# Kernel optimization log

Hardware: AMD Instinct MI355X
Metric: run time of the kernel (lower is better)

The kernel has to match this reference:

```python
import jax, jax.numpy as jnp
import numpy as np

N = 30000          # num nodes
E = 480000         # num edges (avg degree 16)
K = 3              # Chebyshev filter order
IN = 128           # input feature dim
LAMBDA_MAX = 2.0   # PyG default spectral bound
DIMS = [IN, 16, 32, 64, 128, 256, 512]


def setup_inputs() -> dict:
    key = jax.random.key(0)
    ks = jax.random.split(key, 20)
    inp = {
        "x": jax.random.normal(ks[0], (N, IN), dtype=jnp.float32),
        "edge_index": jax.random.randint(ks[1], (2, E), 0, N, dtype=jnp.int32),
        "edge_weight": jax.random.uniform(ks[2], (E,), dtype=jnp.float32),
        "batch": jnp.arange(N, dtype=jnp.int32),  # each node its own graph -> pooling is identity
    }
    for i in range(6):
        fi, fo = DIMS[i], DIMS[i + 1]
        scale = 1.0 / np.sqrt(fi * K)
        inp[f"W{i+1}"] = jax.random.normal(ks[3 + 2 * i], (K, fi, fo), dtype=jnp.float32) * scale
        inp[f"b{i+1}"] = jnp.zeros((fo,), dtype=jnp.float32)
    inp["fc_w"] = jax.random.normal(ks[16], (512, 3), dtype=jnp.float32) * 0.05
    inp["fc_b"] = jnp.zeros((3,), dtype=jnp.float32)
    return inp


def _cheb_conv(x, row, col, w_off, diag, W, b):
    """ChebConv with rw-normalized, rescaled Laplacian Lhat = 2L/lmax - I.
    Lhat @ v = scatter(w_off * v[row] -> col) + diag * v."""
    def lmv(v):
        return jax.ops.segment_sum(w_off[:, None] * v[row], col, num_segments=N) + diag * v
    Tx0 = x
    out = Tx0 @ W[0]
    Tx1 = lmv(x)
    out = out + Tx1 @ W[1]
    for k in range(2, W.shape[0]):
        Tx2 = 2.0 * lmv(Tx1) - Tx0
        out = out + Tx2 @ W[k]
        Tx0, Tx1 = Tx1, Tx2
    return out + b


def _forward(x, edge_index, edge_weight, batch, Ws, bs, fc_w, fc_b):
    row, col = edge_index[0], edge_index[1]
    # random-walk Laplacian L = I - D^{-1} A, then Lhat = 2L/lmax - I
    deg = jax.ops.segment_sum(edge_weight, row, num_segments=N)
    deg_inv = jnp.where(deg > 0, 1.0 / deg, 0.0)
    w_off = -(2.0 / LAMBDA_MAX) * deg_inv[row] * edge_weight   # off-diagonal entries of Lhat
    diag = 2.0 / LAMBDA_MAX - 1.0                               # diagonal entry of Lhat (0 for lmax=2)
    h = x
    for W, b in zip(Ws, bs):
        h = _cheb_conv(h, row, col, w_off, diag, W, b)
        h = jax.ops.segment_max(h, batch, num_segments=N)  # global_max_pool; identity since batch=arange
        h = jax.nn.softplus(h)
    return h @ fc_w + fc_b


def reference(x, edge_index, edge_weight, batch, W1, b1, W2, b2, W3, b3, W4, b4, W5, b5, W6, b6, fc_w, fc_b):
    Ws = [W1, W2, W3, W4, W5, W6]
    bs = [b1, b2, b3, b4, b5, b6]
    return _forward(x, edge_index, edge_weight, batch, Ws, bs, fc_w, fc_b)
```

## Files before the change

### kernel.cpp

```cpp
#include <hip/hip_runtime.h>
#include <math.h>
#include <stdint.h>

#define NN 30000
#define EE 480000
#define MPAD 30080
#define SCAN_B 30

typedef __attribute__((ext_vector_type(8))) short short8;
typedef __attribute__((ext_vector_type(4))) float floatx4;

__device__ __forceinline__ float b2f(ushort u) {
    union { uint u; float f; } c; c.u = ((uint)u) << 16; return c.f;
}
__device__ __forceinline__ ushort f2b(float f) {
    union { float f; uint u; } c; c.f = f;
    uint u = c.u;
    uint r = (u + 0x7FFFu + ((u >> 16) & 1u)) >> 16;
    return (ushort)r;
}
__device__ __forceinline__ float softplus_f(float x) {
    float a = fabsf(x) * 1.44269504f;
    float t = __builtin_amdgcn_exp2f(-a);
    float l = __builtin_amdgcn_logf(1.f + t);
    return fmaxf(x, 0.f) + 0.69314718f * l;
}

__device__ __forceinline__ void gld_lds16(const void* g, void* lds) {
    __builtin_amdgcn_global_load_lds(
        (__attribute__((address_space(1))) void*)(uintptr_t)(g),
        (__attribute__((address_space(3))) void*)(uint32_t)(uintptr_t)(lds),
        16, 0, 0);
}

__global__ void edge_pass1(const int* __restrict__ row, const int* __restrict__ col,
                           const float* __restrict__ ew,
                           float* __restrict__ deg, int* __restrict__ counts, int E) {
    int e = blockIdx.x * blockDim.x + threadIdx.x;
    if (e >= E) return;
    atomicAdd(&deg[row[e]], ew[e]);
    atomicAdd(&counts[col[e]], 1);
}

__global__ __launch_bounds__(256) void scan_part(const int* __restrict__ counts,
                                                 int* __restrict__ bsums, int N) {
    __shared__ int s[256];
    int t = threadIdx.x;
    int base = blockIdx.x * 1024 + t * 4;
    int4 v = make_int4(0, 0, 0, 0);
    if (base + 3 < N) v = *(const int4*)(counts + base);
    else {
        if (base + 0 < N) v.x = counts[base + 0];
        if (base + 1 < N) v.y = counts[base + 1];
        if (base + 2 < N) v.z = counts[base + 2];
        if (base + 3 < N) v.w = counts[base + 3];
    }
    s[t] = v.x + v.y + v.z + v.w;
    __syncthreads();
    for (int off = 1; off < 256; off <<= 1) {
        int x = (t >= off) ? s[t - off] : 0;
        __syncthreads();
        s[t] += x;
        __syncthreads();
    }
    if (t == 255) bsums[blockIdx.x] = s[255];
}

__global__ void scan_tops(int* __restrict__ bsums) {
    int lane = threadIdx.x & 63;
    int orig = (lane < SCAN_B) ? bsums[lane] : 0;
    int v = orig;
    #pragma unroll
    for (int off = 1; off < 64; off <<= 1) {
        int x = __shfl_up(v, off);
        if (lane >= off) v += x;
    }
    if (lane < SCAN_B) bsums[lane] = v - orig;
}

__global__ __launch_bounds__(256) void scan_final(
        const int* __restrict__ counts, const int* __restrict__ bsums,
        int* __restrict__ offs, int* __restrict__ cursor, int N) {
    __shared__ int s[256];
    int t = threadIdx.x;
    int base = blockIdx.x * 1024 + t * 4;
    int4 v = make_int4(0, 0, 0, 0);
    if (base + 3 < N) v = *(const int4*)(counts + base);
    else {
        if (base + 0 < N) v.x = counts[base + 0];
        if (base + 1 < N) v.y = counts[base + 1];
        if (base + 2 < N) v.z = counts[base + 2];
        if (base + 3 < N) v.w = counts[base + 3];
    }
    int sum = v.x + v.y + v.z + v.w;
    s[t] = sum;
    __syncthreads();
    for (int off = 1; off < 256; off <<= 1) {
        int x = (t >= off) ? s[t - off] : 0;
        __syncthreads();
        s[t] += x;
        __syncthreads();
    }
    int tb = s[t] - sum + bsums[blockIdx.x];
    int4 o;
    o.x = tb;
    o.y = o.x + v.x;
    o.z = o.y + v.y;
    o.w = o.z + v.z;
    if (base + 3 < N) {
        *(int4*)(offs + base) = o;
        *(int4*)(cursor + base) = o;
    } else {
        if (base + 0 < N) { offs[base + 0] = o.x; cursor[base + 0] = o.x; }
        if (base + 1 < N) { offs[base + 1] = o.y; cursor[base + 1] = o.y; }
        if (base + 2 < N) { offs[base + 2] = o.z; cursor[base + 2] = o.z; }
        if (base + 3 < N) { offs[base + 3] = o.w; cursor[base + 3] = o.w; }
    }
    if (blockIdx.x == 0 && t == 0) offs[N] = EE;
}

__global__ void edge_pass2(const int* __restrict__ row, const int* __restrict__ col,
                           const float* __restrict__ ew, const float* __restrict__ deg,
                           int* __restrict__ cursor,
                           int* __restrict__ csr_row, float* __restrict__ csr_w, int E) {
    int e = blockIdx.x * blockDim.x + threadIdx.x;
    if (e >= E) return;
    int r = row[e];
    float d = deg[r];
    float wv = (d > 0.f) ? (-ew[e] / d) : 0.f;
    int pos = atomicAdd(&cursor[col[e]], 1);
    csr_row[pos] = r;
    csr_w[pos] = wv;
}

__global__ void copy_x_kernel(const float* __restrict__ x, ushort* __restrict__ out,
                              int total4) {
    int idx = blockIdx.x * blockDim.x + threadIdx.x;
    if (idx >= total4) return;
    float4 v = *(const float4*)(x + idx * 4);
    ushort4 o;
    o.x = f2b(v.x); o.y = f2b(v.y); o.z = f2b(v.z); o.w = f2b(v.w);
    *(ushort4*)(out + idx * 4) = o;
}

__global__ void wconv_all(const float* __restrict__ W1, const float* __restrict__ W2,
                          const float* __restrict__ W3, const float* __restrict__ W4,
                          const float* __restrict__ W5, const float* __restrict__ W6,
                          ushort* __restrict__ B1, ushort* __restrict__ B2,
                          ushort* __restrict__ B3, ushort* __restrict__ B4,
                          ushort* __restrict__ B5, ushort* __restrict__ B6) {
    int idx = blockIdx.x * blockDim.x + threadIdx.x;
    if (idx < 6144) {
        int row = idx >> 7, k = idx & 127;
        int j = row >> 4, n = row & 15;
        B1[idx] = f2b(W1[(j * 128 + k) * 16 + n]);
    } else if (idx < 8192) {
        int t = idx - 6144; int n = t >> 6, k = t & 63;
        B2[t] = f2b(k < 48 ? W2[k * 32 + n] : 0.f);
    } else if (idx < 14336) {
        int t = idx - 8192; int n = t / 96, k = t - n * 96;
        B3[t] = f2b(W3[k * 64 + n]);
    } else if (idx < 38912) {
        int t = idx - 14336; int n = t / 192, k = t - n * 192;
        B4[t] = f2b(W4[k * 128 + n]);
    } else if (idx < 137216) {
        int t = idx - 38912; int n = t / 384, k = t - n * 384;
        B5[t] = f2b(W5[k * 256 + n]);
    } else if (idx < 530432) {
        int t = idx - 137216; int n = t / 768, k = t - n * 768;
        B6[t] = f2b(W6[k * 512 + n]);
    }
}

template <int FI>
__global__ __launch_bounds__(256) void lmv_bf16(
        const ushort* __restrict__ A, ushort* __restrict__ Out,
        const ushort* __restrict__ Sub, int ldi, int ldo,
        const int* __restrict__ offs, const int* __restrict__ rows,
        const float* __restrict__ w, float scale, int N) {
    constexpr int NPW = 64 / FI;
    int wave = threadIdx.x >> 6;
    int lane = threadIdx.x & 63;
    int sub = lane / FI;
    int fbase = lane & (FI - 1);
    int node = blockIdx.x * (4 * NPW) + wave * NPW + sub;
    if (node >= N) return;
    int e0 = offs[node], e1 = offs[node + 1];
    float acc[4];
    #pragma unroll
    for (int c = 0; c < 4; ++c) acc[c] = 0.f;
    int e = e0;
    for (; e + 4 <= e1; e += 4) {
        int r0 = rows[e], r1 = rows[e + 1], r2 = rows[e + 2], r3 = rows[e + 3];
        float w0 = w[e], w1 = w[e + 1], w2 = w[e + 2], w3 = w[e + 3];
        acc[0] += w0 * b2f(A[(size_t)r0 * ldi + fbase]);
        acc[1] += w1 * b2f(A[(size_t)r1 * ldi + fbase]);
        acc[2] += w2 * b2f(A[(size_t)r2 * ldi + fbase]);
        acc[3] += w3 * b2f(A[(size_t)r3 * ldi + fbase]);
    }
    for (; e < e1; ++e)
        acc[0] += w[e] * b2f(A[(size_t)rows[e] * ldi + fbase]);
    float a = (acc[0] + acc[1]) + (acc[2] + acc[3]);
    ushort* o = Out + (size_t)node * ldo + fbase;
    if (Sub) {
        const ushort* s = Sub + (size_t)node * ldo + fbase;
        *o = f2b(scale * a - b2f(*s));
    } else {
        *o = f2b(scale * a);
    }
}

__global__ __launch_bounds__(256) void lmv_l1_final(
        const ushort* __restrict__ Z,
        const ushort* __restrict__ Y,
        const float* __restrict__ b,
        ushort* __restrict__ Out,
        const int* __restrict__ offs, const int* __restrict__ rows,
        const float* __restrict__ w, int N) {
    int wave = threadIdx.x >> 6;
    int lane = threadIdx.x & 63;
    int sub = lane >> 4, f = lane & 15;
    int node = blockIdx.x * 16 + wave * 4 + sub;
    if (node >= N) return;
    int e0 = offs[node], e1 = offs[node + 1];
    const ushort* Z2 = Z + 16;
    float acc[4];
    #pragma unroll
    for (int c = 0; c < 4; ++c) acc[c] = 0.f;
    int e = e0;
    for (; e + 4 <= e1; e += 4) {
        int r0 = rows[e], r1 = rows[e + 1], r2 = rows[e + 2], r3 = rows[e + 3];
        float w0 = w[e], w1 = w[e + 1], w2 = w[e + 2], w3 = w[e + 3];
        acc[0] += w0 * b2f(Z2[(size_t)r0 * 32 + f]);
        acc[1] += w1 * b2f(Z2[(size_t)r1 * 32 + f]);
        acc[2] += w2 * b2f(Z2[(size_t)r2 * 32 + f]);
        acc[3] += w3 * b2f(Z2[(size_t)r3 * 32 + f]);
    }
    for (; e < e1; ++e)
        acc[0] += w[e] * b2f(Z2[(size_t)rows[e] * 32 + f]);
    float z3 = (acc[0] + acc[1]) + (acc[2] + acc[3]);
    float y0 = b2f(Y[(size_t)node * 48 + f]);
    float y2 = b2f(Y[(size_t)node * 48 + 32 + f]);
    float z1 = b2f(Z[(size_t)node * 32 + f]);
    float v = y0 + z1 + 2.f * z3 - y2 + b[f];
    Out[(size_t)node * 64 + f] = f2b(softplus_f(v));
}

template <int VEC>
__global__ __launch_bounds__(256) void lmv_vec(
        const ushort* __restrict__ A, ushort* __restrict__ Out,
        const ushort* __restrict__ Sub, int ld,
        const int* __restrict__ offs, const int* __restrict__ rows,
        const float* __restrict__ w, float scale) {
    constexpr int CH = 8;
    int node = blockIdx.x * 4 + (threadIdx.x >> 6);
    int lane = threadIdx.x & 63;
    int fbase = lane * VEC;
    int e0 = __builtin_amdgcn_readfirstlane(offs[node]);
    int e1 = __builtin_amdgcn_readfirstlane(offs[node + 1]);
    float acc[CH][VEC];
    #pragma unroll
    for (int c = 0; c < CH; ++c)
        #pragma unroll
        for (int v = 0; v < VEC; ++v) acc[c][v] = 0.f;
    int e = e0;
    for (; e + CH <= e1; e += CH) {
        #pragma unroll
        for (int c = 0; c < CH; ++c) {
            int r = rows[e + c];
            float we = w[e + c];
            const ushort* pr = A + (size_t)r * ld + fbase;
            if constexpr (VEC == 4) {
                ushort4 u = *(const ushort4*)pr;
                acc[c][0] += we * b2f(u.x); acc[c][1] += we * b2f(u.y);
                acc[c][2] += we * b2f(u.z); acc[c][3] += we * b2f(u.w);
            } else if constexpr (VEC == 2) {
                ushort2 u = *(const ushort2*)pr;
                acc[c][0] += we * b2f(u.x); acc[c][1] += we * b2f(u.y);
            } else {
                acc[c][0] += we * b2f(*pr);
            }
        }
    }
    for (; e < e1; ++e) {
        int c = e & (CH - 1);
        int r = rows[e];
        float we = w[e];
        const ushort* pr = A + (size_t)r * ld + fbase;
        if constexpr (VEC == 4) {
            ushort4 u = *(const ushort4*)pr;
            acc[c][0] += we * b2f(u.x); acc[c][1] += we * b2f(u.y);
            acc[c][2] += we * b2f(u.z); acc[c][3] += we * b2f(u.w);
        } else if constexpr (VEC == 2) {
            ushort2 u = *(const ushort2*)pr;
            acc[c][0] += we * b2f(u.x); acc[c][1] += we * b2f(u.y);
        } else {
            acc[c][0] += we * b2f(*pr);
        }
    }
    #pragma unroll
    for (int c = 1; c < CH; ++c)
        #pragma unroll
        for (int v = 0; v < VEC; ++v) acc[0][v] += acc[c][v];
    ushort* o = Out + (size_t)node * ld + fbase;
    if (Sub) {
        const ushort* s = Sub + (size_t)node * ld + fbase;
        ushort tmp[VEC];
        #pragma unroll
        for (int v = 0; v < VEC; ++v) tmp[v] = f2b(scale * acc[0][v] - b2f(s[v]));
        #pragma unroll
        for (int v = 0; v < VEC; ++v) o[v] = tmp[v];
    } else {
        #pragma unroll
        for (int v = 0; v < VEC; ++v) o[v] = f2b(scale * acc[0][v]);
    }
}

template <int BN, bool ACT = true>
__global__ __launch_bounds__(256) void gemm_mfma(
        const ushort* __restrict__ A, int lda, int K,
        const ushort* __restrict__ Bt,
        const float* __restrict__ bias,
        ushort* __restrict__ Out, int ldo) {
    constexpr int BM = 128, BK = 32;
    constexpr int WR = 4;
    constexpr int SM = BM / WR;
    constexpr int SN = BN;
    constexpr int FM = SM / 16;
    constexpr int FN = SN / 16;
    constexpr int CB = BN / 16;
    __shared__ __align__(16) ushort As[BM][BK];
    __shared__ __align__(16) ushort Bs[BN][BK];
    int tid = threadIdx.x;
    int wv = tid >> 6, ln = tid & 63;
    int q = ln >> 4, r16 = ln & 15;
    int m0 = blockIdx.x * BM;

    int lrow = ln >> 2;
    int gseg = (ln & 3) ^ ((ln >> 3) & 3);
    const ushort* Abase = A + (size_t)(m0 + lrow) * lda + gseg * 8;
    const ushort* Bbase = Bt + (size_t)lrow * K + gseg * 8;

    floatx4 acc[FM][FN];
    #pragma unroll
    for (int i = 0; i < FM; ++i)
        #pragma unroll
        for (int j = 0; j < FN; ++j) acc[i][j] = (floatx4){0.f, 0.f, 0.f, 0.f};

    int sw = (q ^ ((r16 >> 1) & 3)) * 8;
    int aoff[FM], boff[FN];
    #pragma unroll
    for (int i = 0; i < FM; ++i) aoff[i] = (wv * SM + i * 16 + r16) * BK + sw;
    #pragma unroll
    for (int j = 0; j < FN; ++j) boff[j] = (j * 16 + r16) * BK + sw;
    const ushort* ldsA = &As[0][0];
    const ushort* ldsB = &Bs[0][0];

    for (int k0 = 0; k0 < K; k0 += BK) {
        gld_lds16(Abase + (size_t)(wv * 16) * lda + k0, &As[wv * 16][0]);
        gld_lds16(Abase + (size_t)(64 + wv * 16) * lda + k0, &As[64 + wv * 16][0]);
        if constexpr (CB == 4) {
            gld_lds16(Bbase + (size_t)(wv * 16) * K + k0, &Bs[wv * 16][0]);
        } else {
            if (wv < CB) gld_lds16(Bbase + (size_t)(wv * 16) * K + k0, &Bs[wv * 16][0]);
        }
        __syncthreads();
        short8 af[FM], bf[FN];
        #pragma unroll
        for (int i = 0; i < FM; ++i) af[i] = *(const short8*)(ldsA + aoff[i]);
        #pragma unroll
        for (int j = 0; j < FN; ++j) bf[j] = *(const short8*)(ldsB + boff[j]);
        #pragma unroll
        for (int i = 0; i < FM; ++i)
            #pragma unroll
            for (int j = 0; j < FN; ++j)
                acc[i][j] = __builtin_amdgcn_mfma_f32_16x16x32_bf16(
                    af[i], bf[j], acc[i][j], 0, 0, 0);
        __syncthreads();
    }
    #pragma unroll
    for (int i = 0; i < FM; ++i) {
        #pragma unroll
        for (int j = 0; j < FN; ++j) {
            int n = j * 16 + r16;
            float bv = ACT ? bias[n] : 0.f;
            #pragma unroll
            for (int r = 0; r < 4; ++r) {
                int m = m0 + wv * SM + i * 16 + q * 4 + r;
                float v = acc[i][j][r] + bv;
                Out[(size_t)m * ldo + n] = f2b(ACT ? softplus_f(v) : v);
            }
        }
    }
}

template <bool FC = false, int YB = 0>
__global__ __launch_bounds__(256) void gemm_bk64(
        const ushort* __restrict__ A, int lda, int K,
        const ushort* __restrict__ Bt,
        const float* __restrict__ bias,
        ushort* __restrict__ Out, int ldo,
        const float* __restrict__ fcw, float* __restrict__ fcout) {
    constexpr int BM = 128, BN = 128, BK = 64;
    __shared__ __align__(16) ushort As[BM][BK];
    __shared__ __align__(16) ushort Bs[BN][BK];
    int tid = threadIdx.x;
    int wv = tid >> 6, ln = tid & 63;
    int wm = wv & 1, wn = wv >> 1;
    int q = ln >> 4, r16 = ln & 15;
    int yb = blockIdx.x & ((1 << YB) - 1);
    int xb = blockIdx.x >> YB;
    int m0 = xb * BM;
    int n0 = yb * BN;

    int lrow8 = ln >> 3, slds = ln & 7;
    int gseg = slds ^ lrow8;
    const ushort* Abase = A + (size_t)(m0 + lrow8) * lda + gseg * 8;
    const ushort* Bbase = Bt + (size_t)(n0 + lrow8) * K + gseg * 8;

    floatx4 acc[4][4];
    #pragma unroll
    for (int i = 0; i < 4; ++i)
        #pragma unroll
        for (int j = 0; j < 4; ++j) acc[i][j] = (floatx4){0.f, 0.f, 0.f, 0.f};

    int r7 = r16 & 7;
    int aoff[2][4], boff[2][4];
    #pragma unroll
    for (int s = 0; s < 2; ++s) {
        int segp = ((s * 4 + q) ^ r7) * 8;
        #pragma unroll
        for (int i = 0; i < 4; ++i) {
            aoff[s][i] = (wm * 64 + i * 16 + r16) * BK + segp;
            boff[s][i] = (wn * 64 + i * 16 + r16) * BK + segp;
        }
    }
    const ushort* ldsA = &As[0][0];
    const ushort* ldsB = &Bs[0][0];

    for (int k0 = 0; k0 < K; k0 += BK) {
        #pragma unroll
        for (int g = 0; g < 4; ++g)
            gld_lds16(Abase + (size_t)(wv * 8 + g * 32) * lda + k0,
                      &As[wv * 8 + g * 32][0]);
        #pragma unroll
        for (int g = 0; g < 4; ++g)
            gld_lds16(Bbase + (size_t)(wv * 8 + g * 32) * K + k0,
                      &Bs[wv * 8 + g * 32][0]);
        __syncthreads();
        #pragma unroll
        for (int s = 0; s < 2; ++s) {
            short8 af[4], bf[4];
            #pragma unroll
            for (int i = 0; i < 4; ++i) af[i] = *(const short8*)(ldsA + aoff[s][i]);
            #pragma unroll
            for (int j = 0; j < 4; ++j) bf[j] = *(const short8*)(ldsB + boff[s][j]);
            #pragma unroll
            for (int i = 0; i < 4; ++i)
                #pragma unroll
                for (int j = 0; j < 4; ++j)
                    acc[i][j] = __builtin_amdgcn_mfma_f32_16x16x32_bf16(
                        af[i], bf[j], acc[i][j], 0, 0, 0);
        }
        __syncthreads();
    }

    if constexpr (FC) {
        int pb = yb * 2 + wn;
        #pragma unroll
        for (int i = 0; i < 4; ++i) {
            #pragma unroll
            for (int r = 0; r < 4; ++r) {
                float p0 = 0.f, p1 = 0.f, p2 = 0.f;
                #pragma unroll
                for (int j = 0; j < 4; ++j) {
                    int n = n0 + wn * 64 + j * 16 + r16;
                    float v = softplus_f(acc[i][j][r] + bias[n]);
                    p0 += v * fcw[n * 3 + 0];
                    p1 += v * fcw[n * 3 + 1];
                    p2 += v * fcw[n * 3 + 2];
                }
                #pragma unroll
                for (int off = 1; off < 16; off <<= 1) {
                    p0 += __shfl_xor(p0, off);
                    p1 += __shfl_xor(p1, off);
                    p2 += __shfl_xor(p2, off);
                }
                if (r16 == 0) {
                    int m = m0 + wm * 64 + i * 16 + q * 4 + r;
                    float* dst = fcout + ((size_t)pb * MPAD + m) * 3;
                    dst[0] = p0; dst[1] = p1; dst[2] = p2;
                }
            }
        }
    } else {
        #pragma unroll
        for (int i = 0; i < 4; ++i) {
            #pragma unroll
            for (int j = 0; j < 4; ++j) {
                int n = n0 + wn * 64 + j * 16 + r16;
                float bv = bias[n];
                #pragma unroll
                for (int r = 0; r < 4; ++r) {
                    int m = m0 + wm * 64 + i * 16 + q * 4 + r;
                    Out[(size_t)m * ldo + n] = f2b(softplus_f(acc[i][j][r] + bv));
                }
            }
        }
    }
}

__global__ __launch_bounds__(256) void fc_reduce(
        const float* __restrict__ part, const float* __restrict__ fcb,
        float* __restrict__ out) {
    int idx = blockIdx.x * blockDim.x + threadIdx.x;
    if (idx >= NN * 3) return;
    int c = idx - (idx / 3) * 3;
    float s = 0.f;
    #pragma unroll
    for (int pb = 0; pb < 8; ++pb)
        s += part[(size_t)pb * MPAD * 3 + idx];
    out[idx] = s + fcb[c];
}

static inline size_t align256(size_t x) { return (x + 255) & ~(size_t)255; }

extern "C" void kernel_launch(void* const* d_in, const int* in_sizes, int n_in,
                              void* d_out, int out_size, void* d_ws, size_t ws_size,
                              hipStream_t stream) {
    const float* x   = (const float*)d_in[0];
    const int*   ei  = (const int*)d_in[1];
    const float* ew  = (const float*)d_in[2];
    const float* W[6]  = { (const float*)d_in[4],  (const float*)d_in[6],
                           (const float*)d_in[8],  (const float*)d_in[10],
                           (const float*)d_in[12], (const float*)d_in[14] };
    const float* Bv[6] = { (const float*)d_in[5],  (const float*)d_in[7],
                           (const float*)d_in[9],  (const float*)d_in[11],
                           (const float*)d_in[13], (const float*)d_in[15] };
    const float* fc_w = (const float*)d_in[16];
    const float* fc_b = (const float*)d_in[17];
    float* out = (float*)d_out;

    const int* e_row = ei;
    const int* e_col = ei + EE;

    const int fi_arr[5]   = { 16, 32, 64, 128, 256 };
    const int fo_arr[5]   = { 32, 64, 128, 256, 512 };
    const int Kpad_arr[5] = { 64, 96, 192, 384, 768 };
    const int ldo_arr[5]  = { 96, 192, 384, 768, 512 };

    char* p = (char*)d_ws;
    float* deg    = (float*)p; p += align256((size_t)NN * 4);
    int*   counts = (int*)p;   p += align256((size_t)NN * 4);
    int*   offs   = (int*)p;   p += align256((size_t)(NN + 1) * 4);
    int*   cursor = (int*)p;   p += align256((size_t)NN * 4);
    int*   bsums  = (int*)p;   p += align256((size_t)SCAN_B * 4);
    int*   csr_r  = (int*)p;   p += align256((size_t)EE * 4);
    float* csr_w  = (float*)p; p += align256((size_t)EE * 4);
    ushort* Bt1   = (ushort*)p; p += align256((size_t)48 * 128 * 2);
    ushort* Bt[5];
    for (int L = 0; L < 5; ++L) {
        Bt[L] = (ushort*)p;
        p += align256((size_t)fo_arr[L] * Kpad_arr[L] * 2);
    }
    float* fcpart = (float*)p; p += align256((size_t)8 * MPAD * 3 * 4);
    ushort* xb   = (ushort*)p; p += align256((size_t)MPAD * 128 * 2);
    ushort* Ybuf = (ushort*)p; p += align256((size_t)MPAD * 48 * 2);
    ushort* Zbuf = (ushort*)p; p += align256((size_t)MPAD * 32 * 2);
    ushort* buf0 = (ushort*)p; p += align256((size_t)MPAD * 768 * 2);
    ushort* buf1 = (ushort*)p; p += align256((size_t)MPAD * 768 * 2);
    (void)ws_size; (void)n_in; (void)in_sizes; (void)out_size;

    hipMemsetAsync(deg, 0, align256((size_t)NN * 4) + (size_t)NN * 4, stream);

    {
        int blocks = (EE + 255) / 256;
        edge_pass1<<<blocks, 256, 0, stream>>>(e_row, e_col, ew, deg, counts, EE);
        scan_part<<<SCAN_B, 256, 0, stream>>>(counts, bsums, NN);
        scan_tops<<<1, 64, 0, stream>>>(bsums);
        scan_final<<<SCAN_B, 256, 0, stream>>>(counts, bsums, offs, cursor, NN);
        edge_pass2<<<blocks, 256, 0, stream>>>(e_row, e_col, ew, deg, cursor, csr_r, csr_w, EE);
    }

    wconv_all<<<(530432 + 255) / 256, 256, 0, stream>>>(
        W[0], W[1], W[2], W[3], W[4], W[5],
        Bt1, Bt[0], Bt[1], Bt[2], Bt[3], Bt[4]);

    copy_x_kernel<<<(NN * 128 / 4 + 255) / 256, 256, 0, stream>>>(x, xb, NN * 128 / 4);

    gemm_mfma<48, false><<<dim3(MPAD / 128), 256, 0, stream>>>(
        xb, 128, 128, Bt1, nullptr, Ybuf, 48);
    lmv_bf16<32><<<(NN + 7) / 8, 256, 0, stream>>>(
        Ybuf + 16, Zbuf, nullptr, 48, 32, offs, csr_r, csr_w, 1.0f, NN);
    lmv_l1_final<<<(NN + 15) / 16, 256, 0, stream>>>(
        Zbuf, Ybuf, Bv[0], buf1, offs, csr_r, csr_w, NN);

    ushort* Abuf[5] = { buf1, buf0, buf1, buf0, buf1 };
    ushort* Obuf[5] = { buf0, buf1, buf0, buf1, buf0 };

    for (int L = 0; L < 5; ++L) {
        int fi = fi_arr[L];
        int ldA = Kpad_arr[L];
        int ldO = ldo_arr[L];
        ushort* A = Abuf[L];
        ushort* O = Obuf[L];

        switch (fi) {
            case 16:
                lmv_bf16<16><<<(NN + 15) / 16, 256, 0, stream>>>(
                    A, A + fi, nullptr, ldA, ldA, offs, csr_r, csr_w, 1.0f, NN);
                lmv_bf16<16><<<(NN + 15) / 16, 256, 0, stream>>>(
                    A + fi, A + 2 * fi, A, ldA, ldA, offs, csr_r, csr_w, 2.0f, NN);
                break;
            case 32:
                lmv_bf16<32><<<(NN + 7) / 8, 256, 0, stream>>>(
                    A, A + fi, nullptr, ldA, ldA, offs, csr_r, csr_w, 1.0f, NN);
                lmv_bf16<32><<<(NN + 7) / 8, 256, 0, stream>>>(
                    A + fi, A + 2 * fi, A, ldA, ldA, offs, csr_r, csr_w, 2.0f, NN);
                break;
            case 64:
                lmv_vec<1><<<NN / 4, 256, 0, stream>>>(
                    A, A + fi, nullptr, ldA, offs, csr_r, csr_w, 1.0f);
                lmv_vec<1><<<NN / 4, 256, 0, stream>>>(
                    A + fi, A + 2 * fi, A, ldA, offs, csr_r, csr_w, 2.0f);
                break;
            case 128:
                lmv_vec<2><<<NN / 4, 256, 0, stream>>>(
                    A, A + fi, nullptr, ldA, offs, csr_r, csr_w, 1.0f);
                lmv_vec<2><<<NN / 4, 256, 0, stream>>>(
                    A + fi, A + 2 * fi, A, ldA, offs, csr_r, csr_w, 2.0f);
                break;
            default:
                lmv_vec<4><<<NN / 4, 256, 0, stream>>>(
                    A, A + fi, nullptr, ldA, offs, csr_r, csr_w, 1.0f);
                lmv_vec<4><<<NN / 4, 256, 0, stream>>>(
                    A + fi, A + 2 * fi, A, ldA, offs, csr_r, csr_w, 2.0f);
                break;
        }

        int K = Kpad_arr[L];
        switch (fo_arr[L]) {
            case 32:
                gemm_mfma<32><<<dim3(MPAD / 128), 256, 0, stream>>>(
                    A, ldA, K, Bt[L], Bv[L + 1], O, ldO);
                break;
            case 64:
                gemm_mfma<64><<<dim3(MPAD / 128), 256, 0, stream>>>(
                    A, ldA, K, Bt[L], Bv[L + 1], O, ldO);
                break;
            case 128:
                gemm_bk64<false, 0><<<dim3(MPAD / 128), 256, 0, stream>>>(
                    A, ldA, K, Bt[L], Bv[L + 1], O, ldO, nullptr, nullptr);
                break;
            case 256:
                gemm_bk64<false, 1><<<dim3(MPAD / 128 * 2), 256, 0, stream>>>(
                    A, ldA, K, Bt[L], Bv[L + 1], O, ldO, nullptr, nullptr);
                break;
            default:
                gemm_bk64<true, 2><<<dim3(MPAD / 128 * 4), 256, 0, stream>>>(
                    A, ldA, K, Bt[L], Bv[L + 1], nullptr, 0, fc_w, fcpart);
                break;
        }
    }

    fc_reduce<<<(NN * 3 + 255) / 256, 256, 0, stream>>>(fcpart, fc_b, out);
}
```

Baseline: 489.2 us.

## Double-buffer LDS tiles in MFMA GEMMs and widen lmv edge unroll

Both MFMA GEMM kernels now keep two LDS buffers and issue the direct-to-LDS global loads for the next K tile before computing the current one. Raw s_barrier and s_waitcnt vmcnt control when each tile is consumed, so load latency can overlap with MFMA work. The sparse Laplacian kernel also accumulates 16 edges per chunk instead of 8, giving more loads in flight. In exchange, LDS use doubles, register pressure rises, and correctness depends on the hand-counted vmcnt values matching the compiler's instruction emission.

New measurement: 909.3 us. 85.9% more time.

```diff
diff --git a/kernel.cpp b/kernel.cpp
--- a/kernel.cpp
+++ b/kernel.cpp
@@ -31,6 +31,18 @@
         (__attribute__((address_space(1))) void*)(uintptr_t)(g),
         (__attribute__((address_space(3))) void*)(uint32_t)(uintptr_t)(lds),
         16, 0, 0);
+}
+
+__device__ __forceinline__ void barrier_raw() {
+    __asm__ volatile("s_barrier" ::: "memory");
+}
+template <int N>
+__device__ __forceinline__ void waitcnt_vm() {
+    if constexpr (N == 0) __asm__ volatile("s_waitcnt vmcnt(0)" ::: "memory");
+    else if constexpr (N == 2) __asm__ volatile("s_waitcnt vmcnt(2)" ::: "memory");
+    else if constexpr (N == 3) __asm__ volatile("s_waitcnt vmcnt(3)" ::: "memory");
+    else if constexpr (N == 4) __asm__ volatile("s_waitcnt vmcnt(4)" ::: "memory");
+    else if constexpr (N == 8) __asm__ volatile("s_waitcnt vmcnt(8)" ::: "memory");
 }
 
 __global__ void edge_pass1(const int* __restrict__ row, const int* __restrict__ col,
@@ -252,7 +264,7 @@
         const ushort* __restrict__ Sub, int ld,
         const int* __restrict__ offs, const int* __restrict__ rows,
         const float* __restrict__ w, float scale) {
-    constexpr int CH = 8;
+    constexpr int CH = 16;
     int node = blockIdx.x * 4 + (threadIdx.x >> 6);
     int lane = threadIdx.x & 63;
     int fbase = lane * VEC;
@@ -323,14 +335,13 @@
         const float* __restrict__ bias,
         ushort* __restrict__ Out, int ldo) {
     constexpr int BM = 128, BK = 32;
-    constexpr int WR = 4;
-    constexpr int SM = BM / WR;
-    constexpr int SN = BN;
-    constexpr int FM = SM / 16;
-    constexpr int FN = SN / 16;
+    constexpr int SM = 32;
+    constexpr int FM = 2;
+    constexpr int FN = BN / 16;
     constexpr int CB = BN / 16;
-    __shared__ __align__(16) ushort As[BM][BK];
-    __shared__ __align__(16) ushort Bs[BN][BK];
+    constexpr int WAITN = (BN == 64) ? 3 : 2;
+    __shared__ __align__(16) ushort As[2][BM][BK];
+    __shared__ __align__(16) ushort Bs[2][BN][BK];
     int tid = threadIdx.x;
     int wv = tid >> 6, ln = tid & 63;
     int q = ln >> 4, r16 = ln & 15;
@@ -353,18 +364,19 @@
     for (int i = 0; i < FM; ++i) aoff[i] = (wv * SM + i * 16 + r16) * BK + sw;
     #pragma unroll
     for (int j = 0; j < FN; ++j) boff[j] = (j * 16 + r16) * BK + sw;
-    const ushort* ldsA = &As[0][0];
-    const ushort* ldsB = &Bs[0][0];
-
-    for (int k0 = 0; k0 < K; k0 += BK) {
-        gld_lds16(Abase + (size_t)(wv * 16) * lda + k0, &As[wv * 16][0]);
-        gld_lds16(Abase + (size_t)(64 + wv * 16) * lda + k0, &As[64 + wv * 16][0]);
+
+    auto stage = [&](int b, int k0) {
+        gld_lds16(Abase + (size_t)(wv * 16) * lda + k0, &As[b][wv * 16][0]);
+        gld_lds16(Abase + (size_t)(64 + wv * 16) * lda + k0, &As[b][64 + wv * 16][0]);
         if constexpr (CB == 4) {
-            gld_lds16(Bbase + (size_t)(wv * 16) * K + k0, &Bs[wv * 16][0]);
+            gld_lds16(Bbase + (size_t)(wv * 16) * K + k0, &Bs[b][wv * 16][0]);
         } else {
-            if (wv < CB) gld_lds16(Bbase + (size_t)(wv * 16) * K + k0, &Bs[wv * 16][0]);
-        }
-        __syncthreads();
+            if (wv < CB) gld_lds16(Bbase + (size_t)(wv * 16) * K + k0, &Bs[b][wv * 16][0]);
+        }
+    };
+    auto compute = [&](int b) {
+        const ushort* ldsA = &As[b][0][0];
+        const ushort* ldsB = &Bs[b][0][0];
         short8 af[FM], bf[FN];
         #pragma unroll
         for (int i = 0; i < FM; ++i) af[i] = *(const short8*)(ldsA + aoff[i]);
@@ -376,7 +388,21 @@
             for (int j = 0; j < FN; ++j)
                 acc[i][j] = __builtin_amdgcn_mfma_f32_16x16x32_bf16(
                     af[i], bf[j], acc[i][j], 0, 0, 0);
-        __syncthreads();
+    };
+
+    int nIter = K / BK;
+    stage(0, 0);
+    for (int i = 0; i < nIter; ++i) {
+        int cur = i & 1;
+        barrier_raw();
+        if (i + 1 < nIter) {
+            stage(cur ^ 1, (i + 1) * BK);
+            waitcnt_vm<WAITN>();
+        } else {
+            waitcnt_vm<0>();
+        }
+        barrier_raw();
+        compute(cur);
     }
     #pragma unroll
     for (int i = 0; i < FM; ++i) {
@@ -402,8 +428,8 @@
         ushort* __restrict__ Out, int ldo,
         const float* __restrict__ fcw, float* __restrict__ fcout) {
     constexpr int BM = 128, BN = 128, BK = 64;
-    __shared__ __align__(16) ushort As[BM][BK];
-    __shared__ __align__(16) ushort Bs[BN][BK];
+    __shared__ __align__(16) ushort As[2][BM][BK];
+    __shared__ __align__(16) ushort Bs[2][BN][BK];
     int tid = threadIdx.x;
     int wv = tid >> 6, ln = tid & 63;
     int wm = wv & 1, wn = wv >> 1;
@@ -435,19 +461,20 @@
             boff[s][i] = (wn * 64 + i * 16 + r16) * BK + segp;
         }
     }
-    const ushort* ldsA = &As[0][0];
-    const ushort* ldsB = &Bs[0][0];
-
-    for (int k0 = 0; k0 < K; k0 += BK) {
+
+    auto stage = [&](int b, int k0) {
         #pragma unroll
         for (int g = 0; g < 4; ++g)
             gld_lds16(Abase + (size_t)(wv * 8 + g * 32) * lda + k0,
-                      &As[wv * 8 + g * 32][0]);
+                      &As[b][wv * 8 + g * 32][0]);
         #pragma unroll
         for (int g = 0; g < 4; ++g)
             gld_lds16(Bbase + (size_t)(wv * 8 + g * 32) * K + k0,
-                      &Bs[wv * 8 + g * 32][0]);
-        __syncthreads();
+                      &Bs[b][wv * 8 + g * 32][0]);
+    };
+    auto compute = [&](int b) {
+        const ushort* ldsA = &As[b][0][0];
+        const ushort* ldsB = &Bs[b][0][0];
         #pragma unroll
         for (int s = 0; s < 2; ++s) {
             short8 af[4], bf[4];
@@ -462,7 +489,21 @@
                     acc[i][j] = __builtin_amdgcn_mfma_f32_16x16x32_bf16(
                         af[i], bf[j], acc[i][j], 0, 0, 0);
         }
-        __syncthreads();
+    };
+
+    int nIter = K / BK;
+    stage(0, 0);
+    for (int i = 0; i < nIter; ++i) {
+        int cur = i & 1;
+        barrier_raw();
+        if (i + 1 < nIter) {
+            stage(cur ^ 1, (i + 1) * BK);
+            waitcnt_vm<8>();
+        } else {
+            waitcnt_vm<0>();
+        }
+        barrier_raw();
+        compute(cur);
     }
 
     if constexpr (FC) {
```
